# Kernel optimization log

Hardware: AMD Instinct MI355X
Metric: run time of the kernel (lower is better)

Reference implementation:

```python
import jax, jax.numpy as jnp
import numpy as np

L, D, HID, NH, E, K, P, IMG, NC, B = 4, 384, 1536, 6, 8, 2, 16, 224, 1000, 8
S = (IMG // P) ** 2 + 1  # 197 tokens (cls + patches)
EPS = 1e-5


def setup_inputs() -> dict:
    ks = iter(jax.random.split(jax.random.key(0), 32))
    g = lambda shape, s=0.02: jax.random.normal(next(ks), shape, jnp.float32) * s
    pd = 3 * P * P
    return dict(
        x=jax.random.normal(next(ks), (B, 3, IMG, IMG), jnp.float32),
        patch_w=g((pd, D)), patch_b=g((D,)),
        cls_tok=g((1, 1, D)), pos=g((1, S, D)),
        qkv_w=g((L, D, 3 * D)), qkv_b=g((L, 3 * D)),
        proj_w=g((L, D, D)), proj_b=g((L, D)),
        ln1_g=jnp.ones((L, D)), ln1_b=jnp.zeros((L, D)),
        ln2_g=jnp.ones((L, D)), ln2_b=jnp.zeros((L, D)),
        router_w=g((L, D, E)), router_b=g((L, E)),
        w1=g((L, E, D, HID)), b1=g((L, E, HID)),
        w2=g((L, E, HID, D)), b2=g((L, E, D)),
        norm_g=jnp.ones((D,)), norm_b=jnp.zeros((D,)),
        fc_w=g((D, NC)), fc_b=g((NC,)),
    )


def _ln(x, g, b):
    m = x.mean(-1, keepdims=True)
    v = ((x - m) ** 2).mean(-1, keepdims=True)
    return (x - m) * jax.lax.rsqrt(v + EPS) * g + b


def _mha(x, wqkv, bqkv, wo, bo):
    Bx, Sx, Dx = x.shape
    hd = Dx // NH
    qkv = x @ wqkv + bqkv
    q, k, v = jnp.split(qkv, 3, axis=-1)
    q = q.reshape(Bx, Sx, NH, hd)
    k = k.reshape(Bx, Sx, NH, hd)
    v = v.reshape(Bx, Sx, NH, hd)
    att = jnp.einsum('bqhd,bkhd->bhqk', q, k) / jnp.sqrt(jnp.float32(hd))
    att = jax.nn.softmax(att, axis=-1)
    o = jnp.einsum('bhqk,bkhd->bqhd', att, v).reshape(Bx, Sx, Dx)
    return o @ wo + bo


def _moe(x, rw, rb, w1, b1, w2, b2, noise):
    # Faithful to the masked-dense SparseMoE: non-routed experts see zeros,
    # so occupied experts leak expert_j(0)=gelu(b1_j)@W2_j+b2_j to all tokens.
    xf = x.reshape(-1, x.shape[-1])                     # [T, D]
    logits = xf @ rw + rb + noise * 0.01                # noisy gating
    vals, idx = jax.lax.top_k(logits, K)                # [T, K]
    gates = jax.nn.softmax(vals, axis=-1)               # [T, K]
    h = jax.nn.gelu(jnp.einsum('td,edh->teh', xf, w1) + b1[None], approximate=False)
    y = jnp.einsum('teh,ehd->ted', h, w2) + b2[None]    # [T, E, D]
    bias0 = jnp.einsum('eh,ehd->ed', jax.nn.gelu(b1, approximate=False), w2) + b2  # expert_j(0)
    oh = jax.nn.one_hot(idx, E, dtype=xf.dtype)         # [T, K, E]
    occ = (oh.sum(0) > 0).astype(xf.dtype)              # [K, E] slot occupancy (mask.sum()>0)
    bias_sum = occ @ bias0                              # [K, D]
    y_sel = jnp.take_along_axis(y, idx[:, :, None], axis=1)  # [T, K, D]
    out = jnp.einsum('tk,tkd->td', gates, y_sel - bias0[idx] + bias_sum[None])
    return out.reshape(x.shape)


def reference(x, patch_w, patch_b, cls_tok, pos, qkv_w, qkv_b, proj_w, proj_b,
              ln1_g, ln1_b, ln2_g, ln2_b, router_w, router_b,
              w1, b1, w2, b2, norm_g, norm_b, fc_w, fc_b):
    Bx = x.shape[0]
    Hp = IMG // P
    # torch unfold patchify: (B,C,Hp,Wp,p,p) -> (B, N, C*p*p), channel-major features
    patches = x.reshape(Bx, 3, Hp, P, Hp, P).transpose(0, 2, 4, 1, 3, 5).reshape(Bx, Hp * Hp, 3 * P * P)
    t = patches @ patch_w + patch_b
    t = jnp.concatenate([jnp.broadcast_to(cls_tok, (Bx, 1, D)), t], axis=1) + pos
    nkey = jax.random.key(42)
    for l in range(L):
        a = _mha(t, qkv_w[l], qkv_b[l], proj_w[l], proj_b[l])
        t = _ln(t + a, ln1_g[l], ln1_b[l])
        noise = jax.random.normal(jax.random.fold_in(nkey, l), (Bx * S, E), t.dtype)
        m = _moe(t, router_w[l], router_b[l], w1[l], b1[l], w2[l], b2[l], noise)
        t = _ln(t + m, ln2_g[l], ln2_b[l])
    t = _ln(t, norm_g, norm_b)
    return t[:, 0] @ fc_w + fc_b
```

## Files before the change

kernel.cpp:

```cpp
#include <hip/hip_runtime.h>
#include <hip/hip_bf16.h>

constexpr int LYR  = 4;
constexpr int DM   = 384;
constexpr int HIDN = 1536;
constexpr int NHEAD = 6;
constexpr int HDIM = 64;
constexpr int NEXP = 8;
constexpr int SEQ  = 197;
constexpr int BATCH = 8;
constexpr int TOK  = BATCH * SEQ;
constexpr int NCLS = 1000;
constexpr int CAPE = TOK;
constexpr int NPATCH = BATCH * 196;
constexpr float EPSLN = 1e-5f;
constexpr int KP = 40;

typedef __attribute__((ext_vector_type(8))) short short8v;
typedef __attribute__((ext_vector_type(4))) short short4v;
typedef __attribute__((ext_vector_type(4))) float f32x4v;

__host__ __device__ inline void tf2x32(unsigned k0, unsigned k1, unsigned x0, unsigned x1,
                                       unsigned& y0, unsigned& y1) {
  unsigned ks2 = k0 ^ k1 ^ 0x1BD11BDAu;
  unsigned v0 = x0 + k0, v1 = x1 + k1;
#define TFR(r) { v0 += v1; v1 = (v1 << (r)) | (v1 >> (32 - (r))); v1 ^= v0; }
  TFR(13) TFR(15) TFR(26) TFR(6)
  v0 += k1;  v1 += ks2 + 1u;
  TFR(17) TFR(29) TFR(16) TFR(24)
  v0 += ks2; v1 += k0 + 2u;
  TFR(13) TFR(15) TFR(26) TFR(6)
  v0 += k0;  v1 += k1 + 3u;
  TFR(17) TFR(29) TFR(16) TFR(24)
  v0 += k1;  v1 += ks2 + 4u;
  TFR(13) TFR(15) TFR(26) TFR(6)
  v0 += ks2; v1 += k0 + 5u;
#undef TFR
  y0 = v0; y1 = v1;
}

__device__ inline float erfinv32(float x) {
  float w = -log1pf(-x * x);
  float p;
  if (w < 5.f) {
    w -= 2.5f;
    p = 2.81022636e-08f;
    p = fmaf(p, w, 3.43273939e-07f);
    p = fmaf(p, w, -3.5233877e-06f);
    p = fmaf(p, w, -4.39150654e-06f);
    p = fmaf(p, w, 0.00021858087f);
    p = fmaf(p, w, -0.00125372503f);
    p = fmaf(p, w, -0.00417768164f);
    p = fmaf(p, w, 0.246640727f);
    p = fmaf(p, w, 1.50140941f);
  } else {
    w = sqrtf(w) - 3.f;
    p = -0.000200214257f;
    p = fmaf(p, w, 0.000100950558f);
    p = fmaf(p, w, 0.00134934322f);
    p = fmaf(p, w, -0.00367342844f);
    p = fmaf(p, w, 0.00573950773f);
    p = fmaf(p, w, -0.0076224613f);
    p = fmaf(p, w, 0.00943887047f);
    p = fmaf(p, w, 1.00167406f);
    p = fmaf(p, w, 2.83297682f);
  }
  return p * x;
}

__device__ inline float gelu_f(float x) {
  return 0.5f * x * (1.f + erff(x * 0.70710678118654752f));
}

__device__ inline unsigned short bf16_rne(float x) {
  unsigned u = __float_as_uint(x);
  unsigned r = (u + 0x7fffu + ((u >> 16) & 1u)) >> 16;
  return (unsigned short)r;
}
__device__ inline void split2(float x, short& hs, short& ls) {
  unsigned hu = bf16_rne(x);
  float hf = __uint_as_float(hu << 16);
  unsigned lu = bf16_rne(x - hf);
  hs = (short)hu; ls = (short)lu;
}

__global__ __launch_bounds__(256) void convw_kernel(const float* __restrict__ src,
                                                    short* __restrict__ dst,
                                                    int K, int N) {
  const int nchunks = (K >> 5) * (N >> 4);
  const int chunk = blockIdx.x * 4 + (threadIdx.x >> 6);
  if (chunk >= nchunks) return;
  const int lane = threadIdx.x & 63;
  const long eoffS = (long)blockIdx.y * K * N;
  const long eoffD = (long)blockIdx.y * nchunks * 1024;
  const int nc = N >> 4;
  const int kt = chunk / nc, nt = chunk - kt * nc;
  const int n = nt * 16 + (lane & 15);
  const int kb = kt * 32 + (lane >> 4) * 8;
  short8v hv, lv;
#pragma unroll
  for (int j = 0; j < 8; j++) {
    short h, l;
    split2(src[eoffS + (long)(kb + j) * N + n], h, l);
    hv[j] = h; lv[j] = l;
  }
  *(short8v*)&dst[eoffD + (long)chunk * 1024 + lane * 8] = hv;
  *(short8v*)&dst[eoffD + (long)chunk * 1024 + 512 + lane * 8] = lv;
}

template <int KTOT, int NTOT, int MODE>
__global__ __launch_bounds__(256) void gemm_lds_kernel(
    const short* __restrict__ Ah, const short* __restrict__ Al,
    const short* __restrict__ Wf, const float* __restrict__ bias,
    const int* __restrict__ lists, const int* __restrict__ counts,
    float* __restrict__ outF, short* __restrict__ outH, short* __restrict__ outL) {
  constexpr int SPE = NTOT / 64;
  constexpr int NK = KTOT / 32;
  constexpr int PIT = 36;
  const int strip = blockIdx.x;
  int e, c0;
  if (MODE) { e = strip / SPE; c0 = (strip - e * SPE) * 64; }
  else { e = 0; c0 = strip * 64; if (c0 >= NTOT) return; }
  const int m = blockIdx.y;
  const int cnt = MODE ? counts[e] : TOK;
  if (m * 64 >= cnt) return;
  const int rowsM = min(64, cnt - m * 64);
  __shared__ int ent[64];
  __shared__ short sh[2][64 * PIT];
  __shared__ short sl[2][64 * PIT];
  const int tid = threadIdx.x;
  const int w = tid >> 6, lane = tid & 63;
  if (MODE) {
    if (tid < 64) ent[tid] = (tid < rowsM) ? lists[e * CAPE + m * 64 + tid] : -1;
    __syncthreads();
  }
  const int sr = tid >> 2, skq = (tid & 3) * 8;
  bool okr; long arow = 0;
  if (MODE == 0) {
    okr = (sr < rowsM);
    arow = (long)(m * 64 + (okr ? sr : 0)) * KTOT;
  } else {
    const int pid = ent[sr];
    okr = (pid >= 0);
    arow = (long)(okr ? ((MODE == 1) ? (pid >> 1) : pid) : 0) * KTOT;
  }
  const short* W = Wf + (long)e * ((KTOT >> 5) * (NTOT >> 4)) * 1024;
  const int wm = (w >> 1) * 32, wn = (w & 1) * 32;
  f32x4v Cr[2][2] = {};
  short8v ch, cl;
#pragma unroll
  for (int j = 0; j < 8; j++) { ch[j] = 0; cl[j] = 0; }
  if (okr) {
    ch = *(const short8v*)&Ah[arow + skq];
    cl = *(const short8v*)&Al[arow + skq];
  }
#pragma unroll 2
  for (int kt = 0; kt < NK; ++kt) {
    const int cb = kt & 1;
    *(short8v*)&sh[cb][sr * PIT + skq] = ch;
    *(short8v*)&sl[cb][sr * PIT + skq] = cl;
    if (kt + 1 < NK && okr) {
      ch = *(const short8v*)&Ah[arow + (kt + 1) * 32 + skq];
      cl = *(const short8v*)&Al[arow + (kt + 1) * 32 + skq];
    }
    const long wkb = ((long)kt * (NTOT >> 4) + (c0 >> 4) + (wn >> 4)) * 1024;
    short8v wh[2], wl[2];
#pragma unroll
    for (int nt = 0; nt < 2; ++nt) {
      wh[nt] = *(const short8v*)&W[wkb + nt * 1024 + lane * 8];
      wl[nt] = *(const short8v*)&W[wkb + nt * 1024 + 512 + lane * 8];
    }
    __syncthreads();
    short8v bh[2], bl[2];
#pragma unroll
    for (int tt = 0; tt < 2; ++tt) {
      const int trow = wm + tt * 16 + (lane & 15);
      bh[tt] = *(const short8v*)&sh[cb][trow * PIT + (lane >> 4) * 8];
      bl[tt] = *(const short8v*)&sl[cb][trow * PIT + (lane >> 4) * 8];
    }
#pragma unroll
    for (int nt = 0; nt < 2; ++nt) {
#pragma unroll
      for (int tt = 0; tt < 2; ++tt) {
        Cr[tt][nt] = __builtin_amdgcn_mfma_f32_16x16x32_bf16(wh[nt], bh[tt], Cr[tt][nt], 0, 0, 0);
        Cr[tt][nt] = __builtin_amdgcn_mfma_f32_16x16x32_bf16(wh[nt], bl[tt], Cr[tt][nt], 0, 0, 0);
        Cr[tt][nt] = __builtin_amdgcn_mfma_f32_16x16x32_bf16(wl[nt], bh[tt], Cr[tt][nt], 0, 0, 0);
      }
    }
  }
  const int tl = lane & 15;
  const int nq = (lane >> 4) * 4;
#pragma unroll
  for (int tt = 0; tt < 2; ++tt) {
    const int trow = wm + tt * 16 + tl;
    if (trow < rowsM) {
      const long orow = (long)(MODE ? ent[trow] : (m * 64 + trow)) * NTOT;
#pragma unroll
      for (int nt = 0; nt < 2; ++nt) {
        const int n = c0 + wn + nt * 16 + nq;
        const float4 bv = *(const float4*)&bias[(MODE ? e * NTOT : 0) + n];
        float o0 = Cr[tt][nt][0] + bv.x, o1 = Cr[tt][nt][1] + bv.y;
        float o2 = Cr[tt][nt][2] + bv.z, o3 = Cr[tt][nt][3] + bv.w;
        if (MODE == 1) {
          o0 = gelu_f(o0); o1 = gelu_f(o1); o2 = gelu_f(o2); o3 = gelu_f(o3);
          short4v hv, lv; short hs, ls;
          split2(o0, hs, ls); hv[0] = hs; lv[0] = ls;
          split2(o1, hs, ls); hv[1] = hs; lv[1] = ls;
          split2(o2, hs, ls); hv[2] = hs; lv[2] = ls;
          split2(o3, hs, ls); hv[3] = hs; lv[3] = ls;
          *(short4v*)&outH[orow + n] = hv;
          *(short4v*)&outL[orow + n] = lv;
        } else {
          *(float4*)&outF[orow + n] = make_float4(o0, o1, o2, o3);
        }
      }
    }
  }
}

__global__ __launch_bounds__(256) void patch_mfma_kernel(const float* __restrict__ x,
                                                         const short* __restrict__ Wf,
                                                         const float* __restrict__ pb,
                                                         const float* __restrict__ pos,
                                                         float* __restrict__ t,
                                                         short* __restrict__ tfh,
                                                         short* __restrict__ tfl) {
  constexpr int KTOT = 768, NTOT = DM;
  const int rowsM = min(64, NPATCH - (int)blockIdx.x * 64);
  const int c0 = blockIdx.z * 64;
  const int tid = threadIdx.x;
  const int w = tid >> 6, lane = tid & 63;
  __shared__ short xh[64 * KP];
  __shared__ short xl[64 * KP];
  const int sr = tid >> 2, skq = (tid & 3) * 8;
  const bool okr = (sr < rowsM);
  const int p = blockIdx.x * 64 + sr;
  const int pbat = okr ? (p / 196) : 0;
  const int pn = okr ? (p - pbat * 196) : 0;
  const int hp = pn / 14, wp = pn - hp * 14;
  const float* xbase = x + ((long)pbat * 3 * 224 + hp * 16) * 224 + wp * 16;
  const int wm = (w >> 1) * 32, wn = (w & 1) * 32;
  f32x4v Cr[2][2] = {};
  float4 ra = make_float4(0.f, 0.f, 0.f, 0.f), rb = ra;
  if (okr) {
    const int f = skq;
    const int c = f >> 8, py = (f >> 4) & 15, px = f & 15;
    const float* ptr = xbase + ((long)c * 224 + py) * 224 + px;
    ra = *(const float4*)ptr;
    rb = *(const float4*)(ptr + 4);
  }
  for (int kt = 0; kt < KTOT / 32; ++kt) {
    __syncthreads();
    {
      const float v[8] = {ra.x, ra.y, ra.z, ra.w, rb.x, rb.y, rb.z, rb.w};
      short8v hv, lv;
#pragma unroll
      for (int j = 0; j < 8; j++) { short h, l; split2(v[j], h, l); hv[j] = h; lv[j] = l; }
      *(short8v*)&xh[sr * KP + skq] = hv;
      *(short8v*)&xl[sr * KP + skq] = lv;
    }
    if (kt + 1 < KTOT / 32 && okr) {
      const int f = (kt + 1) * 32 + skq;
      const int c = f >> 8, py = (f >> 4) & 15, px = f & 15;
      const float* ptr = xbase + ((long)c * 224 + py) * 224 + px;
      ra = *(const float4*)ptr;
      rb = *(const float4*)(ptr + 4);
    }
    __syncthreads();
    short8v bhv[2], blv[2];
#pragma unroll
    for (int tt = 0; tt < 2; ++tt) {
      const int trow = wm + tt * 16 + (lane & 15);
      bhv[tt] = *(const short8v*)&xh[trow * KP + (lane >> 4) * 8];
      blv[tt] = *(const short8v*)&xl[trow * KP + (lane >> 4) * 8];
    }
    const long wkb = ((long)kt * (NTOT >> 4) + (c0 >> 4) + (wn >> 4)) * 1024;
#pragma unroll
    for (int nt = 0; nt < 2; ++nt) {
      const short8v wh = *(const short8v*)&Wf[wkb + nt * 1024 + lane * 8];
      const short8v wl = *(const short8v*)&Wf[wkb + nt * 1024 + 512 + lane * 8];
#pragma unroll
      for (int tt = 0; tt < 2; ++tt) {
        Cr[tt][nt] = __builtin_amdgcn_mfma_f32_16x16x32_bf16(wh, bhv[tt], Cr[tt][nt], 0, 0, 0);
        Cr[tt][nt] = __builtin_amdgcn_mfma_f32_16x16x32_bf16(wh, blv[tt], Cr[tt][nt], 0, 0, 0);
        Cr[tt][nt] = __builtin_amdgcn_mfma_f32_16x16x32_bf16(wl, bhv[tt], Cr[tt][nt], 0, 0, 0);
      }
    }
  }
  const int tl = lane & 15;
  const int nq = (lane >> 4) * 4;
#pragma unroll
  for (int tt = 0; tt < 2; ++tt) {
    const int trow = wm + tt * 16 + tl;
    if (trow < rowsM) {
      const int r = blockIdx.x * 64 + trow;
      const int b2 = r / 196, n2 = r - b2 * 196;
      const long orow = (long)(b2 * SEQ + 1 + n2) * DM;
#pragma unroll
      for (int nt = 0; nt < 2; ++nt) {
        const int n = c0 + wn + nt * 16 + nq;
        const float4 bv = *(const float4*)&pb[n];
        const float4 pv = *(const float4*)&pos[(1 + n2) * DM + n];
        float o0 = Cr[tt][nt][0] + bv.x + pv.x;
        float o1 = Cr[tt][nt][1] + bv.y + pv.y;
        float o2 = Cr[tt][nt][2] + bv.z + pv.z;
        float o3 = Cr[tt][nt][3] + bv.w + pv.w;
        *(float4*)&t[orow + n] = make_float4(o0, o1, o2, o3);
        short4v hv, lv; short hs, ls;
        split2(o0, hs, ls); hv[0] = hs; lv[0] = ls;
        split2(o1, hs, ls); hv[1] = hs; lv[1] = ls;
        split2(o2, hs, ls); hv[2] = hs; lv[2] = ls;
        split2(o3, hs, ls); hv[3] = hs; lv[3] = ls;
        *(short4v*)&tfh[orow + n] = hv;
        *(short4v*)&tfl[orow + n] = lv;
      }
    }
  }
}

__global__ void cls_pos_kernel(const float* __restrict__ cls, const float* __restrict__ pos,
                               float* __restrict__ t,
                               short* __restrict__ tfh, short* __restrict__ tfl) {
  int b = blockIdx.x, d = threadIdx.x;
  float v = cls[d] + pos[d];
  t[(b * SEQ) * DM + d] = v;
  short hs, ls; split2(v, hs, ls);
  tfh[(b * SEQ) * DM + d] = hs;
  tfl[(b * SEQ) * DM + d] = ls;
}

constexpr int QT = 32;
constexpr int SP = 208;
__global__ __launch_bounds__(256) void attn_tile_kernel(const float* __restrict__ qkv,
                                                        short* __restrict__ afh,
                                                        short* __restrict__ afl) {
  const int bh = blockIdx.x;
  const int b = bh / NHEAD, h = bh % NHEAD;
  const int q0 = blockIdx.y * QT;
  const int nq = min(QT, SEQ - q0);
  __shared__ float Qs[64][QT + 4];
  __shared__ float KV[64][68];
  __shared__ float Ss[QT][SP];
  const int tid = threadIdx.x;
  const int tx = tid & 15, ty = tid >> 4;
  for (int i = tid; i < QT * 16; i += 256) {
    const int q = i >> 4, dq = (i & 15) << 2;
    float4 v = make_float4(0.f, 0.f, 0.f, 0.f);
    if (q < nq) v = *(const float4*)&qkv[(long)(b * SEQ + q0 + q) * 1152 + h * HDIM + dq];
    Qs[dq + 0][q] = v.x; Qs[dq + 1][q] = v.y; Qs[dq + 2][q] = v.z; Qs[dq + 3][q] = v.w;
  }
  for (int kt = 0; kt < 4; ++kt) {
    const int kbase = kt * 64;
    __syncthreads();
    for (int i = tid; i < 64 * 16; i += 256) {
      const int key = i >> 4, dq = (i & 15) << 2;
      float4 v = make_float4(0.f, 0.f, 0.f, 0.f);
      if (kbase + key < SEQ)
        v = *(const float4*)&qkv[(long)(b * SEQ + kbase + key) * 1152 + DM + h * HDIM + dq];
      KV[dq + 0][key] = v.x; KV[dq + 1][key] = v.y; KV[dq + 2][key] = v.z; KV[dq + 3][key] = v.w;
    }
    __syncthreads();
    float acc[2][4] = {};
#pragma unroll 16
    for (int d = 0; d < 64; ++d) {
      const float4 k4 = *(const float4*)&KV[d][tx << 2];
      const float a0 = Qs[d][ty * 2], a1 = Qs[d][ty * 2 + 1];
      const float kk[4] = {k4.x, k4.y, k4.z, k4.w};
#pragma unroll
      for (int j = 0; j < 4; j++) {
        acc[0][j] = fmaf(a0, kk[j], acc[0][j]);
        acc[1][j] = fmaf(a1, kk[j], acc[1][j]);
      }
    }
#pragma unroll
    for (int i = 0; i < 2; i++) {
      float4 o = make_float4(acc[i][0] * 0.125f, acc[i][1] * 0.125f,
                             acc[i][2] * 0.125f, acc[i][3] * 0.125f);
      *(float4*)&Ss[ty * 2 + i][kbase + (tx << 2)] = o;
    }
  }
  __syncthreads();
  {
    const int row = tid >> 3, c = tid & 7;
    float m = -1e30f;
    for (int k = c; k < SEQ; k += 8) m = fmaxf(m, Ss[row][k]);
    m = fmaxf(m, __shfl_xor(m, 1)); m = fmaxf(m, __shfl_xor(m, 2)); m = fmaxf(m, __shfl_xor(m, 4));
    float s = 0.f;
    for (int k = c; k < SEQ; k += 8) { float e2 = __expf(Ss[row][k] - m); Ss[row][k] = e2; s += e2; }
    s += __shfl_xor(s, 1); s += __shfl_xor(s, 2); s += __shfl_xor(s, 4);
    const float inv = 1.f / s;
    for (int k = c; k < SEQ; k += 8) Ss[row][k] *= inv;
  }
  float acc[2][4] = {};
  for (int kt = 0; kt < 4; ++kt) {
    const int kbase = kt * 64;
    const int kend = min(64, SEQ - kbase);
    __syncthreads();
    for (int i = tid; i < 64 * 16; i += 256) {
      const int key = i >> 4, dq = (i & 15) << 2;
      float4 v = make_float4(0.f, 0.f, 0.f, 0.f);
      if (kbase + key < SEQ)
        v = *(const float4*)&qkv[(long)(b * SEQ + kbase + key) * 1152 + 2 * DM + h * HDIM + dq];
      *(float4*)&KV[key][dq] = v;
    }
    __syncthreads();
    for (int k = 0; k < kend; ++k) {
      const float4 v4 = *(const float4*)&KV[k][tx << 2];
      const float p0 = Ss[ty * 2][kbase + k], p1 = Ss[ty * 2 + 1][kbase + k];
      const float vv[4] = {v4.x, v4.y, v4.z, v4.w};
#pragma unroll
      for (int j = 0; j < 4; j++) {
        acc[0][j] = fmaf(p0, vv[j], acc[0][j]);
        acc[1][j] = fmaf(p1, vv[j], acc[1][j]);
      }
    }
  }
#pragma unroll
  for (int i = 0; i < 2; i++) {
    const int row = ty * 2 + i;
    if (row < nq) {
      const long o = (long)(b * SEQ + q0 + row) * DM + h * HDIM + (tx << 2);
      short4v hv, lv; short hs, ls;
      split2(acc[i][0], hs, ls); hv[0] = hs; lv[0] = ls;
      split2(acc[i][1], hs, ls); hv[1] = hs; lv[1] = ls;
      split2(acc[i][2], hs, ls); hv[2] = hs; lv[2] = ls;
      split2(acc[i][3], hs, ls); hv[3] = hs; lv[3] = ls;
      *(short4v*)&afh[o] = hv;
      *(short4v*)&afl[o] = lv;
    }
  }
}

__global__ __launch_bounds__(384) void add_ln_kernel(float* __restrict__ t,
                                                     const float* __restrict__ delta,
                                                     const float* __restrict__ g,
                                                     const float* __restrict__ bta,
                                                     short* __restrict__ tfh,
                                                     short* __restrict__ tfl) {
  int tok = blockIdx.x, d = threadIdx.x;
  float v = t[tok * DM + d] + delta[tok * DM + d];
  float sv = v, sq = v * v;
  for (int off = 32; off > 0; off >>= 1) { sv += __shfl_xor(sv, off); sq += __shfl_xor(sq, off); }
  __shared__ float rs[6], rq[6];
  int w = d >> 6, ln = d & 63;
  if (ln == 0) { rs[w] = sv; rq[w] = sq; }
  __syncthreads();
  float mean = 0.f, ms = 0.f;
#pragma unroll
  for (int i = 0; i < 6; i++) { mean += rs[i]; ms += rq[i]; }
  mean *= (1.f / DM); ms *= (1.f / DM);
  float inv = rsqrtf(ms - mean * mean + EPSLN);
  float y = (v - mean) * inv * g[d] + bta[d];
  t[tok * DM + d] = y;
  short hs, ls; split2(y, hs, ls);
  tfh[tok * DM + d] = hs;
  tfl[tok * DM + d] = ls;
}

__global__ __launch_bounds__(256) void router_logits_kernel(const float* __restrict__ t,
                                                            const float* __restrict__ rw,
                                                            const float* __restrict__ rb,
                                                            unsigned k0, unsigned k1,
                                                            float* __restrict__ gates,
                                                            int* __restrict__ idxb) {
  const int tok = blockIdx.x * 4 + (threadIdx.x >> 6);
  const int lane = threadIdx.x & 63;
  const int e = lane & 7, j = lane >> 3;
  const float* xr = t + tok * DM;
  float acc = 0.f;
  for (int d2 = j * 48; d2 < j * 48 + 48; d2++) acc += xr[d2] * rw[d2 * NEXP + e];
  acc += __shfl_xor(acc, 8);
  acc += __shfl_xor(acc, 16);
  acc += __shfl_xor(acc, 32);
  if (lane < 8) {
    acc += rb[e];
    unsigned i = (unsigned)(tok * NEXP + e);
    unsigned y0, y1;
    tf2x32(k0, k1, 0u, i, y0, y1);
    unsigned bits = y0 ^ y1;
    float f = __uint_as_float(0x3f800000u | (bits >> 9)) - 1.0f;
    const float lo = -0.99999994f;
    float u = f * 2.0f + lo;
    u = fmaxf(lo, u);
    acc += 0.01f * (1.41421356f * erfinv32(u));
  }
  float lg[8];
#pragma unroll
  for (int qq = 0; qq < 8; qq++) lg[qq] = __shfl(acc, qq);
  if (lane == 0) {
    int i0 = 0; float v0 = lg[0];
#pragma unroll
    for (int qq = 1; qq < 8; qq++) if (lg[qq] > v0) { v0 = lg[qq]; i0 = qq; }
    int i1 = -1; float v1 = -1e30f;
#pragma unroll
    for (int qq = 0; qq < 8; qq++) if (qq != i0 && lg[qq] > v1) { v1 = lg[qq]; i1 = qq; }
    float e1 = __expf(v1 - v0);
    float g0 = 1.f / (1.f + e1);
    idxb[tok * 2] = i0; idxb[tok * 2 + 1] = i1;
    gates[tok * 2] = g0; gates[tok * 2 + 1] = 1.f - g0;
  }
}

__global__ __launch_bounds__(1024) void bucket_kernel(const int* __restrict__ idxb,
                                                      int* __restrict__ lists,
                                                      int* __restrict__ counts,
                                                      int* __restrict__ occ) {
  __shared__ int lc[NEXP];
  __shared__ int locc[2 * NEXP];
  const int tid = threadIdx.x;
  if (tid < NEXP) lc[tid] = 0;
  if (tid < 2 * NEXP) locc[tid] = 0;
  __syncthreads();
  for (int i = tid; i < 2 * TOK; i += 1024) {
    const int e = idxb[i];
    const int p = atomicAdd(&lc[e], 1);
    lists[e * CAPE + p] = i;
    locc[(i & 1) * NEXP + e] = 1;
  }
  __syncthreads();
  if (tid < NEXP) counts[tid] = lc[tid];
  if (tid < 2 * NEXP) occ[tid] = locc[tid];
}

__global__ void prep_kernel(const float* __restrict__ b2, float* __restrict__ bias0) {
  int e = blockIdx.x, c = threadIdx.x;
  bias0[e * DM + c] = b2[e * DM + c];
}

__global__ __launch_bounds__(384) void bias0_partial_kernel(const float* __restrict__ b1,
                                                            const float* __restrict__ w2,
                                                            float* __restrict__ bias0) {
  const int e = blockIdx.x, kc = blockIdx.y;
  __shared__ float gb[128];
  const int tid = threadIdx.x;
  if (tid < 128) gb[tid] = gelu_f(b1[e * HIDN + kc * 128 + tid]);
  __syncthreads();
  float acc = 0.f;
  const float* W = w2 + ((long)e * HIDN + kc * 128) * DM + tid;
  for (int j2 = 0; j2 < 128; j2++) acc += gb[j2] * W[(long)j2 * DM];
  atomicAdd(&bias0[e * DM + tid], acc);
}

__global__ __launch_bounds__(384) void bias_sum_kernel(const float* __restrict__ bias0,
                                                       const int* __restrict__ occ,
                                                       float* __restrict__ bias_sum) {
  int k = blockIdx.x, d = threadIdx.x;
  float acc = 0.f;
#pragma unroll
  for (int e = 0; e < NEXP; e++)
    if (occ[k * NEXP + e]) acc += bias0[e * DM + d];
  bias_sum[k * DM + d] = acc;
}

__global__ __launch_bounds__(384) void moe_combine_ln_kernel(float* __restrict__ t,
                                                             const float* __restrict__ ybuf,
                                                             const float* __restrict__ gates,
                                                             const int* __restrict__ idxb,
                                                             const float* __restrict__ bias0,
                                                             const float* __restrict__ bias_sum,
                                                             const float* __restrict__ g,
                                                             const float* __restrict__ bta,
                                                             short* __restrict__ tfh,
                                                             short* __restrict__ tfl) {
  int tok = blockIdx.x, d = threadIdx.x;
  float g0 = gates[tok * 2], g1 = gates[tok * 2 + 1];
  int i0 = idxb[tok * 2], i1 = idxb[tok * 2 + 1];
  float m0 = ybuf[(tok * 2) * DM + d] - bias0[i0 * DM + d] + bias_sum[d];
  float m1 = ybuf[(tok * 2 + 1) * DM + d] - bias0[i1 * DM + d] + bias_sum[DM + d];
  float v = t[tok * DM + d] + g0 * m0 + g1 * m1;
  float sv = v, sq = v * v;
  for (int off = 32; off > 0; off >>= 1) { sv += __shfl_xor(sv, off); sq += __shfl_xor(sq, off); }
  __shared__ float rs[6], rq[6];
  int w = d >> 6, ln = d & 63;
  if (ln == 0) { rs[w] = sv; rq[w] = sq; }
  __syncthreads();
  float mean = 0.f, ms = 0.f;
#pragma unroll
  for (int i = 0; i < 6; i++) { mean += rs[i]; ms += rq[i]; }
  mean *= (1.f / DM); ms *= (1.f / DM);
  float inv = rsqrtf(ms - mean * mean + EPSLN);
  float y = (v - mean) * inv * g[d] + bta[d];
  t[tok * DM + d] = y;
  short hs, ls; split2(y, hs, ls);
  tfh[tok * DM + d] = hs;
  tfl[tok * DM + d] = ls;
}

__global__ __launch_bounds__(256) void final_kernel(const float* __restrict__ t,
                                                    const float* __restrict__ ng,
                                                    const float* __restrict__ nb,
                                                    const float* __restrict__ fw,
                                                    const float* __restrict__ fb,
                                                    float* __restrict__ out) {
  int b = blockIdx.x, chunk = blockIdx.y, tid = threadIdx.x;
  __shared__ float xr[DM];
  __shared__ float rs[4], rq[4];
  const float* row = t + (b * SEQ) * DM;
  float sv = 0.f, sq = 0.f;
  for (int i = tid; i < DM; i += 256) { float x = row[i]; xr[i] = x; sv += x; sq += x * x; }
  for (int off = 32; off > 0; off >>= 1) { sv += __shfl_xor(sv, off); sq += __shfl_xor(sq, off); }
  int w = tid >> 6, ln = tid & 63;
  if (ln == 0) { rs[w] = sv; rq[w] = sq; }
  __syncthreads();
  float mean = (rs[0] + rs[1] + rs[2] + rs[3]) * (1.f / DM);
  float ms = (rq[0] + rq[1] + rq[2] + rq[3]) * (1.f / DM);
  float inv = rsqrtf(ms - mean * mean + EPSLN);
  for (int i = tid; i < DM; i += 256) xr[i] = (xr[i] - mean) * inv * ng[i] + nb[i];
  __syncthreads();
  int c = chunk * 250 + tid;
  if (tid < 250) {
    float acc = fb[c];
    for (int k = 0; k < DM; k++) acc += xr[k] * fw[k * NCLS + c];
    out[b * NCLS + c] = acc;
  }
}

extern "C" void kernel_launch(void* const* d_in, const int* in_sizes, int n_in,
                              void* d_out, int out_size, void* d_ws, size_t ws_size,
                              hipStream_t stream) {
  const float* x       = (const float*)d_in[0];
  const float* patch_w = (const float*)d_in[1];
  const float* patch_b = (const float*)d_in[2];
  const float* cls_tok = (const float*)d_in[3];
  const float* pos     = (const float*)d_in[4];
  const float* qkv_w   = (const float*)d_in[5];
  const float* qkv_b   = (const float*)d_in[6];
  const float* proj_w  = (const float*)d_in[7];
  const float* proj_b  = (const float*)d_in[8];
  const float* ln1_g   = (const float*)d_in[9];
  const float* ln1_b   = (const float*)d_in[10];
  const float* ln2_g   = (const float*)d_in[11];
  const float* ln2_b   = (const float*)d_in[12];
  const float* router_w = (const float*)d_in[13];
  const float* router_b = (const float*)d_in[14];
  const float* w1      = (const float*)d_in[15];
  const float* b1      = (const float*)d_in[16];
  const float* w2      = (const float*)d_in[17];
  const float* b2      = (const float*)d_in[18];
  const float* norm_g  = (const float*)d_in[19];
  const float* norm_b  = (const float*)d_in[20];
  const float* fc_w    = (const float*)d_in[21];
  const float* fc_b    = (const float*)d_in[22];

  float* ws = (float*)d_ws;
  float* t        = ws;
  float* qkv      = t + TOK * DM;
  float* proj     = qkv + TOK * 1152;
  float* ybuf     = proj + TOK * DM;
  float* bias0    = ybuf + TOK * 2 * DM;
  float* bias_sum = bias0 + NEXP * DM;
  float* gates    = bias_sum + 2 * DM;
  int* idxb   = (int*)(gates + TOK * 2);
  int* lists  = idxb + TOK * 2;
  int* counts = lists + NEXP * CAPE;
  int* occ    = counts + NEXP;
  short* tfh = (short*)(occ + 2 * NEXP);
  short* tfl = tfh + TOK * DM;
  short* afh = tfl + TOK * DM;
  short* afl = afh + TOK * DM;
  short* hbh = afl + TOK * DM;
  short* hbl = hbh + 2 * TOK * HIDN;
  short* wqf = hbl + 2 * TOK * HIDN;
  short* wpf = wqf + 864 * 1024;
  short* w1f = wpf + 288 * 1024;
  short* w2f = w1f + 8 * 1152 * 1024;
  short* wpatf = w2f + 8 * 1152 * 1024;

  convw_kernel<<<dim3(144, 1), 256, 0, stream>>>(patch_w, wpatf, 768, DM);
  patch_mfma_kernel<<<dim3(25, 1, 6), 256, 0, stream>>>(x, wpatf, patch_b, pos, t, tfh, tfl);
  cls_pos_kernel<<<BATCH, DM, 0, stream>>>(cls_tok, pos, t, tfh, tfl);

  for (int l = 0; l < LYR; l++) {
    convw_kernel<<<dim3(216, 1), 256, 0, stream>>>(qkv_w + (long)l * DM * 1152, wqf, DM, 1152);
    convw_kernel<<<dim3(72, 1), 256, 0, stream>>>(proj_w + (long)l * DM * DM, wpf, DM, DM);
    convw_kernel<<<dim3(288, NEXP), 256, 0, stream>>>(w1 + (long)l * NEXP * DM * HIDN, w1f, DM, HIDN);
    convw_kernel<<<dim3(288, NEXP), 256, 0, stream>>>(w2 + (long)l * NEXP * HIDN * DM, w2f, HIDN, DM);

    gemm_lds_kernel<DM, 1152, 0><<<dim3(24, 25), 256, 0, stream>>>(
        tfh, tfl, wqf, qkv_b + l * 1152, nullptr, nullptr, qkv, nullptr, nullptr);
    attn_tile_kernel<<<dim3(BATCH * NHEAD, 7), 256, 0, stream>>>(qkv, afh, afl);
    gemm_lds_kernel<DM, DM, 0><<<dim3(8, 25), 256, 0, stream>>>(
        afh, afl, wpf, proj_b + l * DM, nullptr, nullptr, proj, nullptr, nullptr);
    add_ln_kernel<<<TOK, DM, 0, stream>>>(t, proj, ln1_g + l * DM, ln1_b + l * DM, tfh, tfl);

    prep_kernel<<<NEXP, DM, 0, stream>>>(b2 + l * NEXP * DM, bias0);
    bias0_partial_kernel<<<dim3(NEXP, 12), 384, 0, stream>>>(
        b1 + l * NEXP * HIDN, w2 + (long)l * NEXP * HIDN * DM, bias0);
    unsigned kl0, kl1;
    tf2x32(0u, 42u, 0u, (unsigned)l, kl0, kl1);
    router_logits_kernel<<<TOK / 4, 256, 0, stream>>>(
        t, router_w + l * DM * NEXP, router_b + l * NEXP, kl0, kl1, gates, idxb);
    bucket_kernel<<<1, 1024, 0, stream>>>(idxb, lists, counts, occ);
    bias_sum_kernel<<<2, 384, 0, stream>>>(bias0, occ, bias_sum);
    gemm_lds_kernel<DM, HIDN, 1><<<dim3(192, 25), 256, 0, stream>>>(
        tfh, tfl, w1f, b1 + l * NEXP * HIDN, lists, counts, nullptr, hbh, hbl);
    gemm_lds_kernel<HIDN, DM, 2><<<dim3(48, 25), 256, 0, stream>>>(
        hbh, hbl, w2f, b2 + l * NEXP * DM, lists, counts, ybuf, nullptr, nullptr);
    moe_combine_ln_kernel<<<TOK, DM, 0, stream>>>(t, ybuf, gates, idxb, bias0, bias_sum,
                                                  ln2_g + l * DM, ln2_b + l * DM, tfh, tfl);
  }

  final_kernel<<<dim3(BATCH, 4), 256, 0, stream>>>(t, norm_g, norm_b, fc_w, fc_b,
                                                   (float*)d_out);
}
```

Measured before the change: 940.0 us.

## Compute attention with split-bf16 MFMA and emit QKV as bf16 hi/lo pairs

Replaces the fp32 FMA attention kernel with one that computes QK^T and PV using bf16x3 split MFMA instructions. Scores stay in registers, the softmax runs with cross-lane shuffles, and P and V are staged through LDS. The QKV GEMM gains a mode that writes hi/lo bf16 halves directly instead of fp32, so the attention kernel reads pre-split operands. This moves attention from the vector ALU onto the matrix cores, with some precision risk from the three-term split and extra LDS traffic.

```diff
diff --git a/kernel.cpp b/kernel.cpp
--- a/kernel.cpp
+++ b/kernel.cpp
@@ -18,6 +18,7 @@
 
 typedef __attribute__((ext_vector_type(8))) short short8v;
 typedef __attribute__((ext_vector_type(4))) short short4v;
+typedef __attribute__((ext_vector_type(2))) short short2v;
 typedef __attribute__((ext_vector_type(4))) float f32x4v;
 
 __host__ __device__ inline void tf2x32(unsigned k0, unsigned k1, unsigned x0, unsigned x1,
@@ -114,15 +115,17 @@
     const short* __restrict__ Wf, const float* __restrict__ bias,
     const int* __restrict__ lists, const int* __restrict__ counts,
     float* __restrict__ outF, short* __restrict__ outH, short* __restrict__ outL) {
+  constexpr bool ISMOE = (MODE == 1 || MODE == 2);
+  constexpr bool SPLITOUT = (MODE == 1 || MODE == 3);
   constexpr int SPE = NTOT / 64;
   constexpr int NK = KTOT / 32;
   constexpr int PIT = 36;
   const int strip = blockIdx.x;
   int e, c0;
-  if (MODE) { e = strip / SPE; c0 = (strip - e * SPE) * 64; }
+  if (ISMOE) { e = strip / SPE; c0 = (strip - e * SPE) * 64; }
   else { e = 0; c0 = strip * 64; if (c0 >= NTOT) return; }
   const int m = blockIdx.y;
-  const int cnt = MODE ? counts[e] : TOK;
+  const int cnt = ISMOE ? counts[e] : TOK;
   if (m * 64 >= cnt) return;
   const int rowsM = min(64, cnt - m * 64);
   __shared__ int ent[64];
@@ -130,13 +133,13 @@
   __shared__ short sl[2][64 * PIT];
   const int tid = threadIdx.x;
   const int w = tid >> 6, lane = tid & 63;
-  if (MODE) {
+  if (ISMOE) {
     if (tid < 64) ent[tid] = (tid < rowsM) ? lists[e * CAPE + m * 64 + tid] : -1;
     __syncthreads();
   }
   const int sr = tid >> 2, skq = (tid & 3) * 8;
   bool okr; long arow = 0;
-  if (MODE == 0) {
+  if (!ISMOE) {
     okr = (sr < rowsM);
     arow = (long)(m * 64 + (okr ? sr : 0)) * KTOT;
   } else {
@@ -194,15 +197,15 @@
   for (int tt = 0; tt < 2; ++tt) {
     const int trow = wm + tt * 16 + tl;
     if (trow < rowsM) {
-      const long orow = (long)(MODE ? ent[trow] : (m * 64 + trow)) * NTOT;
+      const long orow = (long)(ISMOE ? ent[trow] : (m * 64 + trow)) * NTOT;
 #pragma unroll
       for (int nt = 0; nt < 2; ++nt) {
         const int n = c0 + wn + nt * 16 + nq;
-        const float4 bv = *(const float4*)&bias[(MODE ? e * NTOT : 0) + n];
+        const float4 bv = *(const float4*)&bias[(ISMOE ? e * NTOT : 0) + n];
         float o0 = Cr[tt][nt][0] + bv.x, o1 = Cr[tt][nt][1] + bv.y;
         float o2 = Cr[tt][nt][2] + bv.z, o3 = Cr[tt][nt][3] + bv.w;
-        if (MODE == 1) {
-          o0 = gelu_f(o0); o1 = gelu_f(o1); o2 = gelu_f(o2); o3 = gelu_f(o3);
+        if (SPLITOUT) {
+          if (MODE == 1) { o0 = gelu_f(o0); o1 = gelu_f(o1); o2 = gelu_f(o2); o3 = gelu_f(o3); }
           short4v hv, lv; short hs, ls;
           split2(o0, hs, ls); hv[0] = hs; lv[0] = ls;
           split2(o1, hs, ls); hv[1] = hs; lv[1] = ls;
@@ -329,104 +332,143 @@
   tfl[(b * SEQ) * DM + d] = ls;
 }
 
-constexpr int QT = 32;
-constexpr int SP = 208;
-__global__ __launch_bounds__(256) void attn_tile_kernel(const float* __restrict__ qkv,
+constexpr int APIT = 232;
+constexpr int VPIT = 40;
+__global__ __launch_bounds__(256) void attn_mfma_kernel(const short* __restrict__ qh,
+                                                        const short* __restrict__ ql,
                                                         short* __restrict__ afh,
                                                         short* __restrict__ afl) {
   const int bh = blockIdx.x;
   const int b = bh / NHEAD, h = bh % NHEAD;
-  const int q0 = blockIdx.y * QT;
-  const int nq = min(QT, SEQ - q0);
-  __shared__ float Qs[64][QT + 4];
-  __shared__ float KV[64][68];
-  __shared__ float Ss[QT][SP];
+  const int q0 = blockIdx.y * 64;
   const int tid = threadIdx.x;
-  const int tx = tid & 15, ty = tid >> 4;
-  for (int i = tid; i < QT * 16; i += 256) {
-    const int q = i >> 4, dq = (i & 15) << 2;
-    float4 v = make_float4(0.f, 0.f, 0.f, 0.f);
-    if (q < nq) v = *(const float4*)&qkv[(long)(b * SEQ + q0 + q) * 1152 + h * HDIM + dq];
-    Qs[dq + 0][q] = v.x; Qs[dq + 1][q] = v.y; Qs[dq + 2][q] = v.z; Qs[dq + 3][q] = v.w;
-  }
-  for (int kt = 0; kt < 4; ++kt) {
-    const int kbase = kt * 64;
+  const int w = tid >> 6, lane = tid & 63;
+  const int tl = lane & 15, g = lane >> 4;
+  __shared__ short ph[4][16 * APIT];
+  __shared__ short pl[4][16 * APIT];
+  __shared__ short vsh[64 * VPIT];
+  __shared__ short vsl[64 * VPIT];
+  const long hq = (long)h * HDIM;
+
+  const int qrow = q0 + w * 16 + tl;
+  const long qtok = (long)(b * SEQ + min(qrow, SEQ - 1)) * 1152;
+  short8v qfh[2], qfl[2];
+#pragma unroll
+  for (int s = 0; s < 2; ++s) {
+    qfh[s] = *(const short8v*)&qh[qtok + hq + s * 32 + g * 8];
+    qfl[s] = *(const short8v*)&ql[qtok + hq + s * 32 + g * 8];
+  }
+
+  f32x4v sc[13];
+#pragma unroll
+  for (int n = 0; n < 13; ++n) {
+    f32x4v acc = {};
+    const long ktok = (long)(b * SEQ + min(n * 16 + tl, SEQ - 1)) * 1152;
+#pragma unroll
+    for (int s = 0; s < 2; ++s) {
+      const short8v kh = *(const short8v*)&qh[ktok + DM + hq + s * 32 + g * 8];
+      const short8v kl = *(const short8v*)&ql[ktok + DM + hq + s * 32 + g * 8];
+      acc = __builtin_amdgcn_mfma_f32_16x16x32_bf16(kh, qfh[s], acc, 0, 0, 0);
+      acc = __builtin_amdgcn_mfma_f32_16x16x32_bf16(kh, qfl[s], acc, 0, 0, 0);
+      acc = __builtin_amdgcn_mfma_f32_16x16x32_bf16(kl, qfh[s], acc, 0, 0, 0);
+    }
+    sc[n] = acc;
+  }
+
+  float m = -1e30f;
+#pragma unroll
+  for (int n = 0; n < 13; ++n)
+#pragma unroll
+    for (int j = 0; j < 4; ++j) {
+      const int key = n * 16 + g * 4 + j;
+      float v = sc[n][j] * 0.125f;
+      v = (key < SEQ) ? v : -1e30f;
+      sc[n][j] = v;
+      m = fmaxf(m, v);
+    }
+  m = fmaxf(m, __shfl_xor(m, 16));
+  m = fmaxf(m, __shfl_xor(m, 32));
+  float sum = 0.f;
+#pragma unroll
+  for (int n = 0; n < 13; ++n)
+#pragma unroll
+    for (int j = 0; j < 4; ++j) {
+      float p = __expf(sc[n][j] - m);
+      sc[n][j] = p; sum += p;
+    }
+  sum += __shfl_xor(sum, 16);
+  sum += __shfl_xor(sum, 32);
+  const float inv = 1.f / sum;
+
+  short* prowh = &ph[w][tl * APIT];
+  short* prowl = &pl[w][tl * APIT];
+#pragma unroll
+  for (int n = 0; n < 13; ++n) {
+    short4v hv, lv;
+#pragma unroll
+    for (int j = 0; j < 4; ++j) {
+      short hs, ls; split2(sc[n][j] * inv, hs, ls);
+      hv[j] = hs; lv[j] = ls;
+    }
+    *(short4v*)&prowh[n * 16 + g * 4] = hv;
+    *(short4v*)&prowl[n * 16 + g * 4] = lv;
+  }
+  {
+    short4v z; z[0] = 0; z[1] = 0; z[2] = 0; z[3] = 0;
+    *(short4v*)&prowh[208 + g * 4] = z;
+    *(short4v*)&prowl[208 + g * 4] = z;
+  }
+
+  const int kp = (tid & 15) * 2;
+  const int dg = (tid >> 4) * 4;
+  f32x4v oacc[4] = {};
+  short4v r0h, r0l, r1h, r1l;
+  {
+    const long t0 = (long)(b * SEQ + min(kp, SEQ - 1)) * 1152 + 2 * DM + hq + dg;
+    const long t1 = (long)(b * SEQ + min(kp + 1, SEQ - 1)) * 1152 + 2 * DM + hq + dg;
+    r0h = *(const short4v*)&qh[t0]; r0l = *(const short4v*)&ql[t0];
+    r1h = *(const short4v*)&qh[t1]; r1l = *(const short4v*)&ql[t1];
+  }
+  for (int st = 0; st < 7; ++st) {
     __syncthreads();
-    for (int i = tid; i < 64 * 16; i += 256) {
-      const int key = i >> 4, dq = (i & 15) << 2;
-      float4 v = make_float4(0.f, 0.f, 0.f, 0.f);
-      if (kbase + key < SEQ)
-        v = *(const float4*)&qkv[(long)(b * SEQ + kbase + key) * 1152 + DM + h * HDIM + dq];
-      KV[dq + 0][key] = v.x; KV[dq + 1][key] = v.y; KV[dq + 2][key] = v.z; KV[dq + 3][key] = v.w;
+#pragma unroll
+    for (int jj = 0; jj < 4; ++jj) {
+      short2v h2; h2[0] = r0h[jj]; h2[1] = r1h[jj];
+      short2v l2; l2[0] = r0l[jj]; l2[1] = r1l[jj];
+      *(short2v*)&vsh[(dg + jj) * VPIT + kp] = h2;
+      *(short2v*)&vsl[(dg + jj) * VPIT + kp] = l2;
+    }
+    if (st + 1 < 7) {
+      const int kb = (st + 1) * 32;
+      const long t0 = (long)(b * SEQ + min(kb + kp, SEQ - 1)) * 1152 + 2 * DM + hq + dg;
+      const long t1 = (long)(b * SEQ + min(kb + kp + 1, SEQ - 1)) * 1152 + 2 * DM + hq + dg;
+      r0h = *(const short4v*)&qh[t0]; r0l = *(const short4v*)&ql[t0];
+      r1h = *(const short4v*)&qh[t1]; r1l = *(const short4v*)&ql[t1];
     }
     __syncthreads();
-    float acc[2][4] = {};
-#pragma unroll 16
-    for (int d = 0; d < 64; ++d) {
-      const float4 k4 = *(const float4*)&KV[d][tx << 2];
-      const float a0 = Qs[d][ty * 2], a1 = Qs[d][ty * 2 + 1];
-      const float kk[4] = {k4.x, k4.y, k4.z, k4.w};
-#pragma unroll
-      for (int j = 0; j < 4; j++) {
-        acc[0][j] = fmaf(a0, kk[j], acc[0][j]);
-        acc[1][j] = fmaf(a1, kk[j], acc[1][j]);
-      }
-    }
-#pragma unroll
-    for (int i = 0; i < 2; i++) {
-      float4 o = make_float4(acc[i][0] * 0.125f, acc[i][1] * 0.125f,
-                             acc[i][2] * 0.125f, acc[i][3] * 0.125f);
-      *(float4*)&Ss[ty * 2 + i][kbase + (tx << 2)] = o;
-    }
-  }
-  __syncthreads();
-  {
-    const int row = tid >> 3, c = tid & 7;
-    float m = -1e30f;
-    for (int k = c; k < SEQ; k += 8) m = fmaxf(m, Ss[row][k]);
-    m = fmaxf(m, __shfl_xor(m, 1)); m = fmaxf(m, __shfl_xor(m, 2)); m = fmaxf(m, __shfl_xor(m, 4));
-    float s = 0.f;
-    for (int k = c; k < SEQ; k += 8) { float e2 = __expf(Ss[row][k] - m); Ss[row][k] = e2; s += e2; }
-    s += __shfl_xor(s, 1); s += __shfl_xor(s, 2); s += __shfl_xor(s, 4);
-    const float inv = 1.f / s;
-    for (int k = c; k < SEQ; k += 8) Ss[row][k] *= inv;
-  }
-  float acc[2][4] = {};
-  for (int kt = 0; kt < 4; ++kt) {
-    const int kbase = kt * 64;
-    const int kend = min(64, SEQ - kbase);
-    __syncthreads();
-    for (int i = tid; i < 64 * 16; i += 256) {
-      const int key = i >> 4, dq = (i & 15) << 2;
-      float4 v = make_float4(0.f, 0.f, 0.f, 0.f);
-      if (kbase + key < SEQ)
-        v = *(const float4*)&qkv[(long)(b * SEQ + kbase + key) * 1152 + 2 * DM + h * HDIM + dq];
-      *(float4*)&KV[key][dq] = v;
-    }
-    __syncthreads();
-    for (int k = 0; k < kend; ++k) {
-      const float4 v4 = *(const float4*)&KV[k][tx << 2];
-      const float p0 = Ss[ty * 2][kbase + k], p1 = Ss[ty * 2 + 1][kbase + k];
-      const float vv[4] = {v4.x, v4.y, v4.z, v4.w};
-#pragma unroll
-      for (int j = 0; j < 4; j++) {
-        acc[0][j] = fmaf(p0, vv[j], acc[0][j]);
-        acc[1][j] = fmaf(p1, vv[j], acc[1][j]);
-      }
-    }
-  }
-#pragma unroll
-  for (int i = 0; i < 2; i++) {
-    const int row = ty * 2 + i;
-    if (row < nq) {
-      const long o = (long)(b * SEQ + q0 + row) * DM + h * HDIM + (tx << 2);
+    const short8v pbh = *(const short8v*)&prowh[st * 32 + g * 8];
+    const short8v pbl = *(const short8v*)&prowl[st * 32 + g * 8];
+#pragma unroll
+    for (int dt = 0; dt < 4; ++dt) {
+      const short8v vfh = *(const short8v*)&vsh[(dt * 16 + tl) * VPIT + g * 8];
+      const short8v vfl = *(const short8v*)&vsl[(dt * 16 + tl) * VPIT + g * 8];
+      oacc[dt] = __builtin_amdgcn_mfma_f32_16x16x32_bf16(vfh, pbh, oacc[dt], 0, 0, 0);
+      oacc[dt] = __builtin_amdgcn_mfma_f32_16x16x32_bf16(vfh, pbl, oacc[dt], 0, 0, 0);
+      oacc[dt] = __builtin_amdgcn_mfma_f32_16x16x32_bf16(vfl, pbh, oacc[dt], 0, 0, 0);
+    }
+  }
+
+  if (qrow < SEQ) {
+    const long obase = (long)(b * SEQ + qrow) * DM + hq;
+#pragma unroll
+    for (int dt = 0; dt < 4; ++dt) {
       short4v hv, lv; short hs, ls;
-      split2(acc[i][0], hs, ls); hv[0] = hs; lv[0] = ls;
-      split2(acc[i][1], hs, ls); hv[1] = hs; lv[1] = ls;
-      split2(acc[i][2], hs, ls); hv[2] = hs; lv[2] = ls;
-      split2(acc[i][3], hs, ls); hv[3] = hs; lv[3] = ls;
-      *(short4v*)&afh[o] = hv;
-      *(short4v*)&afl[o] = lv;
+      split2(oacc[dt][0], hs, ls); hv[0] = hs; lv[0] = ls;
+      split2(oacc[dt][1], hs, ls); hv[1] = hs; lv[1] = ls;
+      split2(oacc[dt][2], hs, ls); hv[2] = hs; lv[2] = ls;
+      split2(oacc[dt][3], hs, ls); hv[3] = hs; lv[3] = ls;
+      *(short4v*)&afh[obase + dt * 16 + g * 4] = hv;
+      *(short4v*)&afl[obase + dt * 16 + g * 4] = lv;
     }
   }
 }
@@ -644,8 +686,7 @@
 
   float* ws = (float*)d_ws;
   float* t        = ws;
-  float* qkv      = t + TOK * DM;
-  float* proj     = qkv + TOK * 1152;
+  float* proj     = t + TOK * DM;
   float* ybuf     = proj + TOK * DM;
   float* bias0    = ybuf + TOK * 2 * DM;
   float* bias_sum = bias0 + NEXP * DM;
@@ -658,7 +699,9 @@
   short* tfl = tfh + TOK * DM;
   short* afh = tfl + TOK * DM;
   short* afl = afh + TOK * DM;
-  short* hbh = afl + TOK * DM;
+  short* qvh = afl + TOK * DM;
+  short* qvl = qvh + TOK * 1152;
+  short* hbh = qvl + TOK * 1152;
   short* hbl = hbh + 2 * TOK * HIDN;
   short* wqf = hbl + 2 * TOK * HIDN;
   short* wpf = wqf + 864 * 1024;
@@ -676,9 +719,9 @@
     convw_kernel<<<dim3(288, NEXP), 256, 0, stream>>>(w1 + (long)l * NEXP * DM * HIDN, w1f, DM, HIDN);
     convw_kernel<<<dim3(288, NEXP), 256, 0, stream>>>(w2 + (long)l * NEXP * HIDN * DM, w2f, HIDN, DM);
 
-    gemm_lds_kernel<DM, 1152, 0><<<dim3(24, 25), 256, 0, stream>>>(
-        tfh, tfl, wqf, qkv_b + l * 1152, nullptr, nullptr, qkv, nullptr, nullptr);
-    attn_tile_kernel<<<dim3(BATCH * NHEAD, 7), 256, 0, stream>>>(qkv, afh, afl);
+    gemm_lds_kernel<DM, 1152, 3><<<dim3(24, 25), 256, 0, stream>>>(
+        tfh, tfl, wqf, qkv_b + l * 1152, nullptr, nullptr, nullptr, qvh, qvl);
+    attn_mfma_kernel<<<dim3(BATCH * NHEAD, 4), 256, 0, stream>>>(qvh, qvl, afh, afl);
     gemm_lds_kernel<DM, DM, 0><<<dim3(8, 25), 256, 0, stream>>>(
         afh, afl, wpf, proj_b + l * DM, nullptr, nullptr, proj, nullptr, nullptr);
     add_ln_kernel<<<TOK, DM, 0, stream>>>(t, proj, ln1_g + l * DM, ln1_b + l * DM, tfh, tfl);
```

After: 900.9 us. -4.2%, faster.
